# Optimization experiments

Hardware: AMD Instinct MI355X
Metric: run time of the kernel (lower is better)

Reference implementation:

```python
import jax, jax.numpy as jnp
import numpy as np

SEQ, B, IN, H, L = 512, 64, 128, 256, 6
STDV = 1.0 / (H ** 0.5)


def setup_inputs() -> dict:
    key = jax.random.key(0)
    ks = jax.random.split(key, 7)
    return {
        "x": jax.random.normal(ks[0], (SEQ, B, IN), jnp.float32),
        "h0": jax.random.normal(ks[1], (L, B, H), jnp.float32),
        "w_ih0": jax.random.uniform(ks[2], (3 * H, IN), jnp.float32, -STDV, STDV),
        "w_ih_rest": jax.random.uniform(ks[3], (L - 1, 3 * H, H), jnp.float32, -STDV, STDV),
        "w_hh": jax.random.uniform(ks[4], (L, 3 * H, H), jnp.float32, -STDV, STDV),
        "b_ih": jax.random.uniform(ks[5], (L, 3 * H), jnp.float32, -STDV, STDV),
        "b_hh": jax.random.uniform(ks[6], (L, 3 * H), jnp.float32, -STDV, STDV),
    }


def _gru_layer(x, h0, w_ih, w_hh, b_ih, b_hh):
    # Precompute input-side gate projections for all timesteps: (S, B, 3H)
    xg = jnp.einsum("sbi,gi->sbg", x, w_ih) + b_ih

    def step(h, xg_t):
        hg = h @ w_hh.T + b_hh  # (B, 3H)
        xr, xz, xn = jnp.split(xg_t, 3, axis=-1)
        hr, hz, hn = jnp.split(hg, 3, axis=-1)
        r = jax.nn.sigmoid(xr + hr)
        z = jax.nn.sigmoid(xz + hz)
        n = jnp.tanh(xn + r * hn)
        h_new = (1.0 - z) * n + z * h
        return h_new, h_new

    h_n, ys = jax.lax.scan(step, h0, xg)
    return ys, h_n


def reference(x, h0, w_ih0, w_ih_rest, w_hh, b_ih, b_hh):
    cur = x
    h_finals = []
    for i in range(L):
        w_ih = w_ih0 if i == 0 else w_ih_rest[i - 1]
        cur, h_n = _gru_layer(cur, h0[i], w_ih, w_hh[i], b_ih[i], b_hh[i])
        h_finals.append(h_n)
    return cur, jnp.stack(h_finals, axis=0)
```

## Files before the change

kernel.cpp:

```cpp
#include <hip/hip_runtime.h>

#define SEQ 512
#define BB 64
#define IN_DIM 128
#define HH 256
#define NL 6
#define G3 768
#define SA 520
#define GPL 4
#define MB 16
#define CHUNK 8
#define NSLOT 4

typedef short short8 __attribute__((ext_vector_type(8)));
typedef short short4v __attribute__((ext_vector_type(4)));
typedef float f32x4 __attribute__((ext_vector_type(4)));

#define L0_FRAGS (48*12)
#define LN_FRAGS (48*16)
#define TOT_FRAGS (L0_FRAGS + 5*LN_FRAGS)
#define STREAM_SHORTS ((size_t)TOT_FRAGS*512)
#define FR_SLOT_SH ((size_t)CHUNK*MB*HH)
#define FR_TOTAL_SH ((size_t)5*GPL*NSLOT*FR_SLOT_SH)
#define FLAGS_OFF_B ((STREAM_SHORTS + FR_TOTAL_SH)*2)
#define NFLAG_INTS (16 + 2*NL*GPL*16)

__device__ __forceinline__ short f2bf(float f) {
    unsigned u = __builtin_bit_cast(unsigned, f);
    u += 0x7fffu + ((u >> 16) & 1u);
    return (short)(u >> 16);
}
__device__ __forceinline__ float sigm(float v) { return __fdividef(1.f, 1.f + __expf(-v)); }
__device__ __forceinline__ float tanh_f(float v) { float e = __expf(2.f * v); return 1.f - __fdividef(2.f, e + 1.f); }

__device__ __forceinline__ void spin1(int* p, int target, unsigned long long ddl) {
    if (__hip_atomic_load(p, __ATOMIC_RELAXED, __HIP_MEMORY_SCOPE_AGENT) >= target) return;
    for (;;) {
        __builtin_amdgcn_s_sleep(2);
        if (__hip_atomic_load(p, __ATOMIC_RELAXED, __HIP_MEMORY_SCOPE_AGENT) >= target) return;
        if (__builtin_amdgcn_s_memrealtime() > ddl) return;
    }
}

__global__ __launch_bounds__(256) void prep_frags(
    const float* __restrict__ w_ih0, const float* __restrict__ w_ih_rest,
    const float* __restrict__ w_hh, short* __restrict__ stream)
{
    int id = blockIdx.x * 256 + threadIdx.x;
    if (id >= TOT_FRAGS * 64) return;
    int fid = id >> 6, lane = id & 63;
    int l, rem, KIN;
    if (fid < L0_FRAGS) { l = 0; rem = fid; KIN = IN_DIM; }
    else { int z = fid - L0_FRAGS; l = 1 + z / LN_FRAGS; rem = z - (l - 1) * LN_FRAGS; KIN = HH; }
    int kt = rem / 48, nt = rem % 48;
    int jt = nt / 3, gate = nt - jt * 3;
    int jj = lane & 15, q2 = lane >> 4;
    int row = gate * HH + jt * 16 + jj;
    int k0 = kt * 32 + q2 * 8;
    const float* src;
    if (k0 < KIN) {
        src = (l == 0) ? (w_ih0 + (size_t)row * IN_DIM + k0)
                       : (w_ih_rest + (size_t)(l - 1) * G3 * HH + (size_t)row * HH + k0);
    } else {
        src = w_hh + (size_t)l * G3 * HH + (size_t)row * HH + (k0 - KIN);
    }
    float4 a = *(const float4*)src;
    float4 c = *(const float4*)(src + 4);
    short8 v;
    v[0] = f2bf(a.x); v[1] = f2bf(a.y); v[2] = f2bf(a.z); v[3] = f2bf(a.w);
    v[4] = f2bf(c.x); v[5] = f2bf(c.y); v[6] = f2bf(c.z); v[7] = f2bf(c.w);
    *((short8*)stream + (size_t)fid * 64 + lane) = v;
}

template<int KTL, int KS>
__device__ __forceinline__ void compute_step(const short* sAm, const short8* bs,
                                             int wave, int lane, f32x4* acc)
{
    const int arow = (lane & 15) * SA + ((lane >> 4) * 8);
    const int w6 = wave * 6;
    #pragma unroll
    for (int kt = 0; kt < KTL; ++kt) {
        short8 a = *reinterpret_cast<const short8*>(&sAm[arow + kt * 32]);
        const short8* bp = bs + ((size_t)(kt * 48 + w6) * 64 + lane);
        short8 b0 = bp[0 * 64], b1 = bp[1 * 64], b2 = bp[2 * 64];
        short8 b3 = bp[3 * 64], b4 = bp[4 * 64], b5 = bp[5 * 64];
        acc[0] = __builtin_amdgcn_mfma_f32_16x16x32_bf16(a, b0, acc[0], 0, 0, 0);
        acc[1] = __builtin_amdgcn_mfma_f32_16x16x32_bf16(a, b1, acc[1], 0, 0, 0);
        if (kt < KS) acc[2] = __builtin_amdgcn_mfma_f32_16x16x32_bf16(a, b2, acc[2], 0, 0, 0);
        else         acc[3] = __builtin_amdgcn_mfma_f32_16x16x32_bf16(a, b2, acc[3], 0, 0, 0);
        acc[4] = __builtin_amdgcn_mfma_f32_16x16x32_bf16(a, b3, acc[4], 0, 0, 0);
        acc[5] = __builtin_amdgcn_mfma_f32_16x16x32_bf16(a, b4, acc[5], 0, 0, 0);
        if (kt < KS) acc[6] = __builtin_amdgcn_mfma_f32_16x16x32_bf16(a, b5, acc[6], 0, 0, 0);
        else         acc[7] = __builtin_amdgcn_mfma_f32_16x16x32_bf16(a, b5, acc[7], 0, 0, 0);
    }
}

__global__ __launch_bounds__(512, 1) void gru_persist(
    const float* __restrict__ x, const float* __restrict__ h0,
    const float* __restrict__ b_ih, const float* __restrict__ b_hh,
    float* __restrict__ y, const short* __restrict__ stream,
    short* __restrict__ fring, int* __restrict__ flags)
{
    extern __shared__ short sAm[];
    const int tid = threadIdx.x;
    const unsigned long long ddl = __builtin_amdgcn_s_memrealtime() + 1000000000ull;

    const int xcc = __builtin_amdgcn_s_getreg(20 | (31 << 11)) & 0xf;
    if (xcc >= NL) return;
    __shared__ int s_slot;
    if (tid == 0) s_slot = __hip_atomic_fetch_add(&flags[xcc], 1, __ATOMIC_RELAXED, __HIP_MEMORY_SCOPE_AGENT);
    __syncthreads();
    const int g = s_slot;
    if (g >= GPL) return;

    const int l = xcc;
    const int lane = tid & 63;
    const int wave = tid >> 6;
    const int q = lane >> 4;
    const int jj = lane & 15;
    const int KINC = (l == 0) ? IN_DIM : HH;

    int* seqf  = flags + 16 + (l * GPL + g) * 16;
    int* cseqf = flags + 16 + NL * GPL * 16 + (l * GPL + g) * 16;
    int* seq_prev  = flags + 16 + ((l - 1) * GPL + g) * 16;
    int* cseq_next = flags + 16 + NL * GPL * 16 + ((l + 1) * GPL + g) * 16;

    const short8* bs = (const short8*)stream + (size_t)((l == 0) ? 0 : (L0_FRAGS + (l - 1) * LN_FRAGS)) * 64;

    float hcur[8];
    float bR[2], bZ[2], bNx[2], bNh[2];
    #pragma unroll
    for (int jt2 = 0; jt2 < 2; ++jt2) {
        int j = (2 * wave + jt2) * 16 + jj;
        bR[jt2]  = b_ih[l * G3 + j] + b_hh[l * G3 + j];
        bZ[jt2]  = b_ih[l * G3 + HH + j] + b_hh[l * G3 + HH + j];
        bNx[jt2] = b_ih[l * G3 + 2 * HH + j];
        bNh[jt2] = b_hh[l * G3 + 2 * HH + j];
        #pragma unroll
        for (int r = 0; r < 4; ++r) {
            int b = 4 * q + r;
            float v = h0[((size_t)l * BB + g * MB + b) * HH + j];
            hcur[jt2 * 4 + r] = v;
        }
    }
    for (int i = tid; i < MB * HH; i += 512) {
        int b = i >> 8, j = i & 255;
        sAm[b * SA + KINC + j] = f2bf(h0[((size_t)l * BB + g * MB + b) * HH + j]);
    }

    for (int t = 0; t < SEQ; ++t) {
        if ((t & 7) == 0) {
            if (tid == 0) {
                if (l > 0) spin1(seq_prev, t + CHUNK, ddl);
                if (l < NL - 1 && t >= NSLOT * CHUNK) spin1(cseq_next, t - (NSLOT - 1) * CHUNK, ddl);
            }
            if (wave == 0) __builtin_amdgcn_fence(__ATOMIC_ACQUIRE, "agent");
            __syncthreads();
        }

        const int slot = (t >> 3) & (NSLOT - 1);

        if (l == 0) {
            const float* xt = x + ((size_t)t * BB + g * MB) * IN_DIM;
            int row = tid >> 5, col = (tid & 31) * 4;
            float4 vv = *(const float4*)(xt + row * IN_DIM + col);
            short4v s;
            s[0] = f2bf(vv.x); s[1] = f2bf(vv.y); s[2] = f2bf(vv.z); s[3] = f2bf(vv.w);
            *reinterpret_cast<short4v*>(&sAm[row * SA + col]) = s;
        } else {
            const short* frsrc = fring + (((size_t)((l - 1) * GPL + g) * NSLOT + slot)) * FR_SLOT_SH
                               + (size_t)(t & 7) * MB * HH;
            int row = tid >> 5, col = (tid & 31) * 8;
            short8 v = *(const short8*)&frsrc[row * HH + col];
            *reinterpret_cast<short8*>(&sAm[row * SA + col]) = v;
        }
        __syncthreads();

        f32x4 acc[8] = {};
        if (l == 0) compute_step<12, 4>(sAm, bs, wave, lane, acc);
        else        compute_step<16, 8>(sAm, bs, wave, lane, acc);
        __syncthreads();

        short* frdst = fring + (((size_t)(l * GPL + g) * NSLOT + slot)) * FR_SLOT_SH
                     + (size_t)(t & 7) * MB * HH;
        float* ydst = y + (size_t)t * BB * HH + (size_t)g * MB * HH;
        #pragma unroll
        for (int jt2 = 0; jt2 < 2; ++jt2) {
            int j = (2 * wave + jt2) * 16 + jj;
            #pragma unroll
            for (int r = 0; r < 4; ++r) {
                int b = 4 * q + r;
                float ho = hcur[jt2 * 4 + r];
                float rg = sigm(acc[jt2 * 4 + 0][r] + bR[jt2]);
                float zg = sigm(acc[jt2 * 4 + 1][r] + bZ[jt2]);
                float ng = tanh_f(acc[jt2 * 4 + 2][r] + bNx[jt2] + rg * (acc[jt2 * 4 + 3][r] + bNh[jt2]));
                float hn = ng + zg * (ho - ng);
                hcur[jt2 * 4 + r] = hn;
                short hb = f2bf(hn);
                sAm[b * SA + KINC + j] = hb;
                if (l < NL - 1) frdst[b * HH + j] = hb;
                else            ydst[b * HH + j] = hn;
            }
        }
        __syncthreads();

        if ((t & 7) == 7 && tid == 0) {
            if (l < NL - 1)
                __hip_atomic_store(seqf, t + 1, __ATOMIC_RELEASE, __HIP_MEMORY_SCOPE_AGENT);
            if (l > 0)
                __hip_atomic_store(cseqf, t + 1, __ATOMIC_RELEASE, __HIP_MEMORY_SCOPE_AGENT);
        }
    }

    #pragma unroll
    for (int jt2 = 0; jt2 < 2; ++jt2) {
        int j = (2 * wave + jt2) * 16 + jj;
        #pragma unroll
        for (int r = 0; r < 4; ++r) {
            int b = 4 * q + r;
            y[(size_t)SEQ * BB * HH + (size_t)l * BB * HH + (size_t)(g * MB + b) * HH + j] = hcur[jt2 * 4 + r];
        }
    }
}

extern "C" void kernel_launch(void* const* d_in, const int* in_sizes, int n_in,
                              void* d_out, int out_size, void* d_ws, size_t ws_size,
                              hipStream_t stream) {
    (void)in_sizes; (void)n_in; (void)out_size; (void)ws_size;
    const float* x         = (const float*)d_in[0];
    const float* h0        = (const float*)d_in[1];
    const float* w_ih0     = (const float*)d_in[2];
    const float* w_ih_rest = (const float*)d_in[3];
    const float* w_hh      = (const float*)d_in[4];
    const float* b_ih      = (const float*)d_in[5];
    const float* b_hh      = (const float*)d_in[6];
    float* y = (float*)d_out;

    short* wstream = (short*)d_ws;
    short* fring   = wstream + STREAM_SHORTS;
    int*   flags   = (int*)((char*)d_ws + FLAGS_OFF_B);

    (void)hipMemsetAsync(flags, 0, NFLAG_INTS * sizeof(int), stream);
    prep_frags<<<(TOT_FRAGS * 64) / 256, 256, 0, stream>>>(w_ih0, w_ih_rest, w_hh, wstream);
    gru_persist<<<256, 512, 65536, stream>>>(x, h0, b_ih, b_hh, y, wstream, fring, flags);
}
```

Measured before the change: 4.837 ms.

## Split GRU into per-chunk input projection and register/LDS-resident recurrent weights

The input-side gate projection is now computed once per 8-step chunk as a batched MFMA GEMM and written to a global scratch buffer. The per-step recurrence then only multiplies the hidden state by w_hh, whose r/z tiles are kept in registers and whose n tiles sit in swizzled LDS, instead of streaming the full concatenated weight from global memory every step. Blocks drop from 512 to 256 threads. The aim is to shorten the serial per-step critical path, at the cost of heavy register pressure, extra global scratch traffic read back with sc0 loads, and lower occupancy.

```diff
diff --git a/kernel.cpp b/kernel.cpp
--- a/kernel.cpp
+++ b/kernel.cpp
@@ -6,23 +6,24 @@
 #define HH 256
 #define NL 6
 #define G3 768
-#define SA 520
 #define GPL 4
 #define MB 16
 #define CHUNK 8
 #define NSLOT 4
+#define NCH (SEQ/CHUNK)
 
 typedef short short8 __attribute__((ext_vector_type(8)));
-typedef short short4v __attribute__((ext_vector_type(4)));
 typedef float f32x4 __attribute__((ext_vector_type(4)));
 
-#define L0_FRAGS (48*12)
-#define LN_FRAGS (48*16)
-#define TOT_FRAGS (L0_FRAGS + 5*LN_FRAGS)
-#define STREAM_SHORTS ((size_t)TOT_FRAGS*512)
-#define FR_SLOT_SH ((size_t)CHUNK*MB*HH)
-#define FR_TOTAL_SH ((size_t)5*GPL*NSLOT*FR_SLOT_SH)
-#define FLAGS_OFF_B ((STREAM_SHORTS + FR_TOTAL_SH)*2)
+#define L0_F (4*48)
+#define LN_F (8*48)
+#define TOT_F (L0_F + 5*LN_F)
+#define STREAM_SH ((size_t)TOT_F*512)
+#define FR_SLOT 32768
+#define FRING_SH ((size_t)5*GPL*NSLOT*FR_SLOT)
+#define XG_OFF_B ((STREAM_SH + FRING_SH)*2)
+#define XG_CU_FLOATS ((size_t)CHUNK*G3*MB)
+#define FLAGS_OFF_B (XG_OFF_B + (size_t)NL*GPL*XG_CU_FLOATS*4)
 #define NFLAG_INTS (16 + 2*NL*GPL*16)
 
 __device__ __forceinline__ short f2bf(float f) {
@@ -42,28 +43,38 @@
     }
 }
 
+struct F4x4 { f32x4 a, b, c, d; };
+__device__ __forceinline__ F4x4 ld4x4_sc0(const float* p0, const float* p1,
+                                          const float* p2, const float* p3) {
+    F4x4 r;
+    asm volatile(
+        "global_load_dwordx4 %0, %4, off sc0\n\t"
+        "global_load_dwordx4 %1, %5, off sc0\n\t"
+        "global_load_dwordx4 %2, %6, off sc0\n\t"
+        "global_load_dwordx4 %3, %7, off sc0\n\t"
+        "s_waitcnt vmcnt(0)"
+        : "=&v"(r.a), "=&v"(r.b), "=&v"(r.c), "=&v"(r.d)
+        : "v"(p0), "v"(p1), "v"(p2), "v"(p3) : "memory");
+    return r;
+}
+
 __global__ __launch_bounds__(256) void prep_frags(
     const float* __restrict__ w_ih0, const float* __restrict__ w_ih_rest,
-    const float* __restrict__ w_hh, short* __restrict__ stream)
+    short* __restrict__ stream)
 {
     int id = blockIdx.x * 256 + threadIdx.x;
-    if (id >= TOT_FRAGS * 64) return;
+    if (id >= TOT_F * 64) return;
     int fid = id >> 6, lane = id & 63;
-    int l, rem, KIN;
-    if (fid < L0_FRAGS) { l = 0; rem = fid; KIN = IN_DIM; }
-    else { int z = fid - L0_FRAGS; l = 1 + z / LN_FRAGS; rem = z - (l - 1) * LN_FRAGS; KIN = HH; }
+    int l, rem;
+    if (fid < L0_F) { l = 0; rem = fid; }
+    else { int z = fid - L0_F; l = 1 + z / LN_F; rem = z % LN_F; }
     int kt = rem / 48, nt = rem % 48;
-    int jt = nt / 3, gate = nt - jt * 3;
+    int gt = nt >> 4, jt = nt & 15;
     int jj = lane & 15, q2 = lane >> 4;
-    int row = gate * HH + jt * 16 + jj;
+    int row = gt * 256 + jt * 16 + jj;
     int k0 = kt * 32 + q2 * 8;
-    const float* src;
-    if (k0 < KIN) {
-        src = (l == 0) ? (w_ih0 + (size_t)row * IN_DIM + k0)
-                       : (w_ih_rest + (size_t)(l - 1) * G3 * HH + (size_t)row * HH + k0);
-    } else {
-        src = w_hh + (size_t)l * G3 * HH + (size_t)row * HH + (k0 - KIN);
-    }
+    const float* src = (l == 0) ? (w_ih0 + (size_t)row * IN_DIM + k0)
+                                : (w_ih_rest + (size_t)(l - 1) * G3 * HH + (size_t)row * HH + k0);
     float4 a = *(const float4*)src;
     float4 c = *(const float4*)(src + 4);
     short8 v;
@@ -72,36 +83,13 @@
     *((short8*)stream + (size_t)fid * 64 + lane) = v;
 }
 
-template<int KTL, int KS>
-__device__ __forceinline__ void compute_step(const short* sAm, const short8* bs,
-                                             int wave, int lane, f32x4* acc)
+__global__ __launch_bounds__(256, 1) void gru_persist(
+    const float* __restrict__ x, const float* __restrict__ h0,
+    const float* __restrict__ w_hh, const float* __restrict__ b_ih,
+    const float* __restrict__ b_hh, float* __restrict__ y,
+    const short* __restrict__ wstream, short* __restrict__ fring,
+    float* __restrict__ xg, int* __restrict__ flags)
 {
-    const int arow = (lane & 15) * SA + ((lane >> 4) * 8);
-    const int w6 = wave * 6;
-    #pragma unroll
-    for (int kt = 0; kt < KTL; ++kt) {
-        short8 a = *reinterpret_cast<const short8*>(&sAm[arow + kt * 32]);
-        const short8* bp = bs + ((size_t)(kt * 48 + w6) * 64 + lane);
-        short8 b0 = bp[0 * 64], b1 = bp[1 * 64], b2 = bp[2 * 64];
-        short8 b3 = bp[3 * 64], b4 = bp[4 * 64], b5 = bp[5 * 64];
-        acc[0] = __builtin_amdgcn_mfma_f32_16x16x32_bf16(a, b0, acc[0], 0, 0, 0);
-        acc[1] = __builtin_amdgcn_mfma_f32_16x16x32_bf16(a, b1, acc[1], 0, 0, 0);
-        if (kt < KS) acc[2] = __builtin_amdgcn_mfma_f32_16x16x32_bf16(a, b2, acc[2], 0, 0, 0);
-        else         acc[3] = __builtin_amdgcn_mfma_f32_16x16x32_bf16(a, b2, acc[3], 0, 0, 0);
-        acc[4] = __builtin_amdgcn_mfma_f32_16x16x32_bf16(a, b3, acc[4], 0, 0, 0);
-        acc[5] = __builtin_amdgcn_mfma_f32_16x16x32_bf16(a, b4, acc[5], 0, 0, 0);
-        if (kt < KS) acc[6] = __builtin_amdgcn_mfma_f32_16x16x32_bf16(a, b5, acc[6], 0, 0, 0);
-        else         acc[7] = __builtin_amdgcn_mfma_f32_16x16x32_bf16(a, b5, acc[7], 0, 0, 0);
-    }
-}
-
-__global__ __launch_bounds__(512, 1) void gru_persist(
-    const float* __restrict__ x, const float* __restrict__ h0,
-    const float* __restrict__ b_ih, const float* __restrict__ b_hh,
-    float* __restrict__ y, const short* __restrict__ stream,
-    short* __restrict__ fring, int* __restrict__ flags)
-{
-    extern __shared__ short sAm[];
     const int tid = threadIdx.x;
     const unsigned long long ddl = __builtin_amdgcn_s_memrealtime() + 1000000000ull;
 
@@ -118,108 +106,257 @@
     const int wave = tid >> 6;
     const int q = lane >> 4;
     const int jj = lane & 15;
-    const int KINC = (l == 0) ? IN_DIM : HH;
-
-    int* seqf  = flags + 16 + (l * GPL + g) * 16;
-    int* cseqf = flags + 16 + NL * GPL * 16 + (l * GPL + g) * 16;
+
+    int* seqf      = flags + 16 + (l * GPL + g) * 16;
+    int* cseqf     = flags + 16 + NL * GPL * 16 + (l * GPL + g) * 16;
     int* seq_prev  = flags + 16 + ((l - 1) * GPL + g) * 16;
     int* cseq_next = flags + 16 + NL * GPL * 16 + ((l + 1) * GPL + g) * 16;
 
-    const short8* bs = (const short8*)stream + (size_t)((l == 0) ? 0 : (L0_FRAGS + (l - 1) * LN_FRAGS)) * 64;
-
-    float hcur[8];
-    float bR[2], bZ[2], bNx[2], bNh[2];
-    #pragma unroll
-    for (int jt2 = 0; jt2 < 2; ++jt2) {
-        int j = (2 * wave + jt2) * 16 + jj;
-        bR[jt2]  = b_ih[l * G3 + j] + b_hh[l * G3 + j];
-        bZ[jt2]  = b_ih[l * G3 + HH + j] + b_hh[l * G3 + HH + j];
-        bNx[jt2] = b_ih[l * G3 + 2 * HH + j];
-        bNh[jt2] = b_hh[l * G3 + 2 * HH + j];
+    __shared__ short sW[16 * 16 * 256];
+    __shared__ short sHl[16 * 256];
+
+    const float* whh = w_hh + (size_t)l * G3 * HH;
+    short8 Wreg[8][8];
+    #pragma unroll
+    for (int tt = 0; tt < 8; ++tt) {
+        int row = (tt >> 2) * 256 + (4 * wave + (tt & 3)) * 16 + jj;
         #pragma unroll
-        for (int r = 0; r < 4; ++r) {
-            int b = 4 * q + r;
-            float v = h0[((size_t)l * BB + g * MB + b) * HH + j];
-            hcur[jt2 * 4 + r] = v;
-        }
-    }
-    for (int i = tid; i < MB * HH; i += 512) {
+        for (int kt = 0; kt < 8; ++kt) {
+            const float* p = whh + (size_t)row * HH + kt * 32 + q * 8;
+            float4 a = *(const float4*)p;
+            float4 c = *(const float4*)(p + 4);
+            short8 v;
+            v[0] = f2bf(a.x); v[1] = f2bf(a.y); v[2] = f2bf(a.z); v[3] = f2bf(a.w);
+            v[4] = f2bf(c.x); v[5] = f2bf(c.y); v[6] = f2bf(c.z); v[7] = f2bf(c.w);
+            Wreg[tt][kt] = v;
+        }
+    }
+    #pragma unroll
+    for (int tb = 0; tb < 4; ++tb) {
+        int row = 512 + (4 * wave + tb) * 16 + jj;
+        #pragma unroll
+        for (int kt = 0; kt < 8; ++kt) {
+            const float* p = whh + (size_t)row * HH + kt * 32 + q * 8;
+            float4 a = *(const float4*)p;
+            float4 c = *(const float4*)(p + 4);
+            short8 v;
+            v[0] = f2bf(a.x); v[1] = f2bf(a.y); v[2] = f2bf(a.z); v[3] = f2bf(a.w);
+            v[4] = f2bf(c.x); v[5] = f2bf(c.y); v[6] = f2bf(c.z); v[7] = f2bf(c.w);
+            int kbyte = kt * 64 + q * 16;
+            *(short8*)((char*)sW + (wave * 4 + tb) * 8192 + jj * 512 + (kbyte ^ ((jj & 7) << 4))) = v;
+        }
+    }
+
+    float biasv[12], bhn[4];
+    #pragma unroll
+    for (int tt = 0; tt < 12; ++tt) {
+        int gt = tt >> 2;
+        int j = (4 * wave + (tt & 3)) * 16 + jj;
+        biasv[tt] = (gt < 2) ? (b_ih[l * G3 + gt * 256 + j] + b_hh[l * G3 + gt * 256 + j])
+                             : b_ih[l * G3 + 512 + j];
+    }
+    #pragma unroll
+    for (int jt2 = 0; jt2 < 4; ++jt2)
+        bhn[jt2] = b_hh[l * G3 + 512 + (4 * wave + jt2) * 16 + jj];
+
+    float hcur[16];
+    #pragma unroll
+    for (int jt2 = 0; jt2 < 4; ++jt2) {
+        int j = (4 * wave + jt2) * 16 + jj;
+        #pragma unroll
+        for (int r = 0; r < 4; ++r)
+            hcur[jt2 * 4 + r] = h0[((size_t)l * BB + g * MB + 4 * q + r) * HH + j];
+    }
+    for (int i = tid; i < MB * HH; i += 256) {
         int b = i >> 8, j = i & 255;
-        sAm[b * SA + KINC + j] = f2bf(h0[((size_t)l * BB + g * MB + b) * HH + j]);
-    }
-
-    for (int t = 0; t < SEQ; ++t) {
-        if ((t & 7) == 0) {
-            if (tid == 0) {
-                if (l > 0) spin1(seq_prev, t + CHUNK, ddl);
-                if (l < NL - 1 && t >= NSLOT * CHUNK) spin1(cseq_next, t - (NSLOT - 1) * CHUNK, ddl);
+        short hb = f2bf(h0[((size_t)l * BB + g * MB + b) * HH + j]);
+        *(short*)((char*)sHl + b * 512 + ((2 * j) ^ ((b & 7) << 4))) = hb;
+    }
+    __syncthreads();
+
+    const size_t lbase = (l == 0) ? 0 : (L0_F + (size_t)(l - 1) * LN_F);
+    const int KTp = (l == 0) ? 4 : 8;
+    float* xg_cu = xg + (size_t)(l * GPL + g) * XG_CU_FLOATS;
+
+    for (int c = 0; c < NCH; ++c) {
+        const int t0 = c * CHUNK;
+
+        if (tid == 0) {
+            if (l > 0) spin1(seq_prev, t0 + CHUNK, ddl);
+            if (l < NL - 1 && c >= NSLOT) spin1(cseq_next, t0 - (NSLOT - 1) * CHUNK, ddl);
+        }
+        if (wave == 0) __builtin_amdgcn_fence(__ATOMIC_ACQUIRE, "agent");
+        __syncthreads();
+
+        const short* frsrc = (l > 0)
+            ? fring + (((size_t)(l - 1) * GPL + g) * NSLOT + (c & 3)) * FR_SLOT : nullptr;
+
+        for (int mh = 0; mh < 2; ++mh) {
+            {
+                f32x4 pa[8][4];
+                #pragma unroll
+                for (int tt = 0; tt < 8; ++tt)
+                    #pragma unroll
+                    for (int m4 = 0; m4 < 4; ++m4)
+                        pa[tt][m4] = (f32x4){biasv[tt], biasv[tt], biasv[tt], biasv[tt]};
+                for (int kt = 0; kt < KTp; ++kt) {
+                    short8 af[4];
+                    #pragma unroll
+                    for (int m4 = 0; m4 < 4; ++m4) {
+                        int ts = mh * 4 + m4;
+                        if (l == 0) {
+                            const float* ap = x + (((size_t)(t0 + ts) * BB + g * MB + jj) * IN_DIM + kt * 32 + q * 8);
+                            float4 a1 = *(const float4*)ap;
+                            float4 a2 = *(const float4*)(ap + 4);
+                            short8 v;
+                            v[0] = f2bf(a1.x); v[1] = f2bf(a1.y); v[2] = f2bf(a1.z); v[3] = f2bf(a1.w);
+                            v[4] = f2bf(a2.x); v[5] = f2bf(a2.y); v[6] = f2bf(a2.z); v[7] = f2bf(a2.w);
+                            af[m4] = v;
+                        } else {
+                            af[m4] = *(const short8*)(frsrc + (size_t)(ts * MB + jj) * HH + kt * 32 + q * 8);
+                        }
+                    }
+                    #pragma unroll
+                    for (int tt = 0; tt < 8; ++tt) {
+                        int gt = tt >> 2, jt = 4 * wave + (tt & 3);
+                        short8 bf = *((const short8*)wstream + ((lbase + kt * 48 + gt * 16 + jt) * 64 + lane));
+                        #pragma unroll
+                        for (int m4 = 0; m4 < 4; ++m4)
+                            pa[tt][m4] = __builtin_amdgcn_mfma_f32_16x16x32_bf16(af[m4], bf, pa[tt][m4], 0, 0, 0);
+                    }
+                }
+                #pragma unroll
+                for (int tt = 0; tt < 8; ++tt) {
+                    int gt = tt >> 2, jt = 4 * wave + (tt & 3);
+                    #pragma unroll
+                    for (int m4 = 0; m4 < 4; ++m4) {
+                        int ts = mh * 4 + m4;
+                        *(f32x4*)(xg_cu + ((size_t)ts * G3 + gt * 256 + jt * 16 + jj) * MB + 4 * q) = pa[tt][m4];
+                    }
+                }
             }
-            if (wave == 0) __builtin_amdgcn_fence(__ATOMIC_ACQUIRE, "agent");
+            {
+                f32x4 pb[4][4];
+                #pragma unroll
+                for (int tb = 0; tb < 4; ++tb)
+                    #pragma unroll
+                    for (int m4 = 0; m4 < 4; ++m4)
+                        pb[tb][m4] = (f32x4){biasv[8 + tb], biasv[8 + tb], biasv[8 + tb], biasv[8 + tb]};
+                for (int kt = 0; kt < KTp; ++kt) {
+                    short8 af[4];
+                    #pragma unroll
+                    for (int m4 = 0; m4 < 4; ++m4) {
+                        int ts = mh * 4 + m4;
+                        if (l == 0) {
+                            const float* ap = x + (((size_t)(t0 + ts) * BB + g * MB + jj) * IN_DIM + kt * 32 + q * 8);
+                            float4 a1 = *(const float4*)ap;
+                            float4 a2 = *(const float4*)(ap + 4);
+                            short8 v;
+                            v[0] = f2bf(a1.x); v[1] = f2bf(a1.y); v[2] = f2bf(a1.z); v[3] = f2bf(a1.w);
+                            v[4] = f2bf(a2.x); v[5] = f2bf(a2.y); v[6] = f2bf(a2.z); v[7] = f2bf(a2.w);
+                            af[m4] = v;
+                        } else {
+                            af[m4] = *(const short8*)(frsrc + (size_t)(ts * MB + jj) * HH + kt * 32 + q * 8);
+                        }
+                    }
+                    #pragma unroll
+                    for (int tb = 0; tb < 4; ++tb) {
+                        int jt = 4 * wave + tb;
+                        short8 bf = *((const short8*)wstream + ((lbase + kt * 48 + 2 * 16 + jt) * 64 + lane));
+                        #pragma unroll
+                        for (int m4 = 0; m4 < 4; ++m4)
+                            pb[tb][m4] = __builtin_amdgcn_mfma_f32_16x16x32_bf16(af[m4], bf, pb[tb][m4], 0, 0, 0);
+                    }
+                }
+                #pragma unroll
+                for (int tb = 0; tb < 4; ++tb) {
+                    int jt = 4 * wave + tb;
+                    #pragma unroll
+                    for (int m4 = 0; m4 < 4; ++m4) {
+                        int ts = mh * 4 + m4;
+                        *(f32x4*)(xg_cu + ((size_t)ts * G3 + 512 + jt * 16 + jj) * MB + 4 * q) = pb[tb][m4];
+                    }
+                }
+            }
+        }
+        __syncthreads();
+
+        short* frdst = (l < NL - 1)
+            ? fring + (((size_t)l * GPL + g) * NSLOT + (c & 3)) * FR_SLOT : nullptr;
+        for (int ts = 0; ts < CHUNK; ++ts) {
+            const int jb = 4 * wave * 16 + jj;
+            const float* xr = xg_cu + (size_t)ts * G3 * MB;
+            F4x4 xrv = ld4x4_sc0(xr + (size_t)(jb) * MB + 4 * q,
+                                 xr + (size_t)(jb + 16) * MB + 4 * q,
+                                 xr + (size_t)(jb + 32) * MB + 4 * q,
+                                 xr + (size_t)(jb + 48) * MB + 4 * q);
+            F4x4 xzv = ld4x4_sc0(xr + (size_t)(256 + jb) * MB + 4 * q,
+                                 xr + (size_t)(256 + jb + 16) * MB + 4 * q,
+                                 xr + (size_t)(256 + jb + 32) * MB + 4 * q,
+                                 xr + (size_t)(256 + jb + 48) * MB + 4 * q);
+            F4x4 xnv = ld4x4_sc0(xr + (size_t)(512 + jb) * MB + 4 * q,
+                                 xr + (size_t)(512 + jb + 16) * MB + 4 * q,
+                                 xr + (size_t)(512 + jb + 32) * MB + 4 * q,
+                                 xr + (size_t)(512 + jb + 48) * MB + 4 * q);
+            f32x4 acc[12];
+            acc[0] = xrv.a; acc[1] = xrv.b; acc[2] = xrv.c; acc[3] = xrv.d;
+            acc[4] = xzv.a; acc[5] = xzv.b; acc[6] = xzv.c; acc[7] = xzv.d;
+            acc[8] = (f32x4){0,0,0,0}; acc[9] = (f32x4){0,0,0,0};
+            acc[10] = (f32x4){0,0,0,0}; acc[11] = (f32x4){0,0,0,0};
+
+            #pragma unroll
+            for (int kt = 0; kt < 8; ++kt) {
+                int kbyte = kt * 64 + q * 16;
+                int swz = kbyte ^ ((jj & 7) << 4);
+                short8 af = *(const short8*)((const char*)sHl + jj * 512 + swz);
+                #pragma unroll
+                for (int tt = 0; tt < 8; ++tt)
+                    acc[tt] = __builtin_amdgcn_mfma_f32_16x16x32_bf16(af, Wreg[tt][kt], acc[tt], 0, 0, 0);
+                #pragma unroll
+                for (int tb = 0; tb < 4; ++tb) {
+                    short8 bf = *(const short8*)((const char*)sW + (wave * 4 + tb) * 8192 + jj * 512 + swz);
+                    acc[8 + tb] = __builtin_amdgcn_mfma_f32_16x16x32_bf16(af, bf, acc[8 + tb], 0, 0, 0);
+                }
+            }
             __syncthreads();
-        }
-
-        const int slot = (t >> 3) & (NSLOT - 1);
-
-        if (l == 0) {
-            const float* xt = x + ((size_t)t * BB + g * MB) * IN_DIM;
-            int row = tid >> 5, col = (tid & 31) * 4;
-            float4 vv = *(const float4*)(xt + row * IN_DIM + col);
-            short4v s;
-            s[0] = f2bf(vv.x); s[1] = f2bf(vv.y); s[2] = f2bf(vv.z); s[3] = f2bf(vv.w);
-            *reinterpret_cast<short4v*>(&sAm[row * SA + col]) = s;
-        } else {
-            const short* frsrc = fring + (((size_t)((l - 1) * GPL + g) * NSLOT + slot)) * FR_SLOT_SH
-                               + (size_t)(t & 7) * MB * HH;
-            int row = tid >> 5, col = (tid & 31) * 8;
-            short8 v = *(const short8*)&frsrc[row * HH + col];
-            *reinterpret_cast<short8*>(&sAm[row * SA + col]) = v;
-        }
-        __syncthreads();
-
-        f32x4 acc[8] = {};
-        if (l == 0) compute_step<12, 4>(sAm, bs, wave, lane, acc);
-        else        compute_step<16, 8>(sAm, bs, wave, lane, acc);
-        __syncthreads();
-
-        short* frdst = fring + (((size_t)(l * GPL + g) * NSLOT + slot)) * FR_SLOT_SH
-                     + (size_t)(t & 7) * MB * HH;
-        float* ydst = y + (size_t)t * BB * HH + (size_t)g * MB * HH;
+
+            f32x4 xn4[4] = {xnv.a, xnv.b, xnv.c, xnv.d};
+            float* ydst = y + (size_t)(t0 + ts) * BB * HH;
+            #pragma unroll
+            for (int jt2 = 0; jt2 < 4; ++jt2) {
+                int j = (4 * wave + jt2) * 16 + jj;
+                #pragma unroll
+                for (int r = 0; r < 4; ++r) {
+                    int b = 4 * q + r;
+                    float ho = hcur[jt2 * 4 + r];
+                    float rg = sigm(acc[jt2][r]);
+                    float zg = sigm(acc[4 + jt2][r]);
+                    float ng = tanh_f(xn4[jt2][r] + rg * (acc[8 + jt2][r] + bhn[jt2]));
+                    float hn = ng + zg * (ho - ng);
+                    hcur[jt2 * 4 + r] = hn;
+                    short hb = f2bf(hn);
+                    *(short*)((char*)sHl + b * 512 + ((2 * j) ^ ((b & 7) << 4))) = hb;
+                    if (l < NL - 1) frdst[(size_t)ts * MB * HH + b * HH + j] = hb;
+                    else            ydst[((size_t)g * MB + b) * HH + j] = hn;
+                }
+            }
+            __syncthreads();
+        }
+
+        if (tid == 0) {
+            if (l < NL - 1)
+                __hip_atomic_store(seqf, t0 + CHUNK, __ATOMIC_RELEASE, __HIP_MEMORY_SCOPE_AGENT);
+            if (l > 0)
+                __hip_atomic_store(cseqf, t0 + CHUNK, __ATOMIC_RELEASE, __HIP_MEMORY_SCOPE_AGENT);
+        }
+    }
+
+    #pragma unroll
+    for (int jt2 = 0; jt2 < 4; ++jt2) {
+        int j = (4 * wave + jt2) * 16 + jj;
         #pragma unroll
-        for (int jt2 = 0; jt2 < 2; ++jt2) {
-            int j = (2 * wave + jt2) * 16 + jj;
-            #pragma unroll
-            for (int r = 0; r < 4; ++r) {
-                int b = 4 * q + r;
-                float ho = hcur[jt2 * 4 + r];
-                float rg = sigm(acc[jt2 * 4 + 0][r] + bR[jt2]);
-                float zg = sigm(acc[jt2 * 4 + 1][r] + bZ[jt2]);
-                float ng = tanh_f(acc[jt2 * 4 + 2][r] + bNx[jt2] + rg * (acc[jt2 * 4 + 3][r] + bNh[jt2]));
-                float hn = ng + zg * (ho - ng);
-                hcur[jt2 * 4 + r] = hn;
-                short hb = f2bf(hn);
-                sAm[b * SA + KINC + j] = hb;
-                if (l < NL - 1) frdst[b * HH + j] = hb;
-                else            ydst[b * HH + j] = hn;
-            }
-        }
-        __syncthreads();
-
-        if ((t & 7) == 7 && tid == 0) {
-            if (l < NL - 1)
-                __hip_atomic_store(seqf, t + 1, __ATOMIC_RELEASE, __HIP_MEMORY_SCOPE_AGENT);
-            if (l > 0)
-                __hip_atomic_store(cseqf, t + 1, __ATOMIC_RELEASE, __HIP_MEMORY_SCOPE_AGENT);
-        }
-    }
-
-    #pragma unroll
-    for (int jt2 = 0; jt2 < 2; ++jt2) {
-        int j = (2 * wave + jt2) * 16 + jj;
-        #pragma unroll
-        for (int r = 0; r < 4; ++r) {
-            int b = 4 * q + r;
-            y[(size_t)SEQ * BB * HH + (size_t)l * BB * HH + (size_t)(g * MB + b) * HH + j] = hcur[jt2 * 4 + r];
-        }
+        for (int r = 0; r < 4; ++r)
+            y[(size_t)SEQ * BB * HH + (size_t)l * BB * HH + ((size_t)g * MB + 4 * q + r) * HH + j] = hcur[jt2 * 4 + r];
     }
 }
 
@@ -237,10 +374,12 @@
     float* y = (float*)d_out;
 
     short* wstream = (short*)d_ws;
-    short* fring   = wstream + STREAM_SHORTS;
+    short* fring   = wstream + STREAM_SH;
+    float* xg      = (float*)((char*)d_ws + XG_OFF_B);
     int*   flags   = (int*)((char*)d_ws + FLAGS_OFF_B);
 
     (void)hipMemsetAsync(flags, 0, NFLAG_INTS * sizeof(int), stream);
-    prep_frags<<<(TOT_FRAGS * 64) / 256, 256, 0, stream>>>(w_ih0, w_ih_rest, w_hh, wstream);
-    gru_persist<<<256, 512, 65536, stream>>>(x, h0, b_ih, b_hh, y, wstream, fring, flags);
-}
+    prep_frags<<<(TOT_F * 64) / 256, 256, 0, stream>>>(w_ih0, w_ih_rest, wstream);
+    gru_persist<<<256, 256, 0, stream>>>(x, h0, w_hh, b_ih, b_hh, y,
+                                         wstream, fring, xg, flags);
+}
```

Result: slower. 8.930 ms (+84.6%).
